# Optimization experiments

Hardware: AMD Instinct MI355X
Metric: run time of the kernel (lower is better)

Reference implementation:

```python
import jax, jax.numpy as jnp
import numpy as np

B, N, D, R, K = 16384, 20, 64, 3, 64  # batch, triples per sample, embed dim, n_relations, r_dim


def setup_inputs() -> dict:
    key = jax.random.key(0)
    ks = jax.random.split(key, 8)
    # xavier_normal std for [2D, K] matrices: sqrt(2/(2D+K))
    std_w = float(np.sqrt(2.0 / (2 * D + K)))
    std_r = float(np.sqrt(2.0 / (R + K)))
    return {
        "u_emb": jax.random.normal(ks[0], (B, D), dtype=jnp.float32),
        "i_emb": jax.random.normal(ks[1], (B, D), dtype=jnp.float32),
        "a_emb": jax.random.normal(ks[2], (B, N, D), dtype=jnp.float32),
        "o_emb": jax.random.normal(ks[3], (B, N, D), dtype=jnp.float32),
        "s": jax.random.randint(ks[4], (B, N), 0, R, dtype=jnp.int64),
        "w_uir": jax.random.normal(ks[5], (R, 2 * D, K), dtype=jnp.float32) * std_w,
        "w_aor": jax.random.normal(ks[6], (R, 2 * D, K), dtype=jnp.float32) * std_w,
        "r_vec": jax.random.normal(ks[7], (R, K), dtype=jnp.float32) * std_r,
    }


def reference(u_emb, i_emb, a_emb, o_emb, s, w_uir, w_aor, r_vec):
    # transr predictor, bpr loss
    ui_in = jnp.concatenate([u_emb, i_emb], axis=-1)          # [B, 2D]
    ao_in = jnp.concatenate([a_emb, o_emb], axis=-1)          # [B, N, 2D]
    n_rel = w_uir.shape[0]
    ui_emb = jnp.zeros(ao_in.shape[:2] + (w_uir.shape[-1],), dtype=ui_in.dtype)  # [B, N, K]
    ao_emb = jnp.zeros_like(ui_emb)
    for r_idx in range(n_rel):  # small fixed relation count
        m = (s == r_idx)[..., None]                            # [B, N, 1]
        ui_r = ui_in @ w_uir[r_idx] + r_vec[r_idx]             # [B, K]
        ao_r = jnp.einsum("bnd,dk->bnk", ao_in, w_aor[r_idx])  # [B, N, K]
        ui_emb = jnp.where(m, ui_r[:, None, :], ui_emb)
        ao_emb = jnp.where(m, ao_r, ao_emb)
    pred = jnp.sum(ui_emb * ao_emb, axis=-1)                   # [B, N]
    return pred
```

## Files before the change

kernel.cpp:

```cpp
#include <hip/hip_runtime.h>
#include <hip/hip_bf16.h>

#define BB   16384
#define NN   20
#define NREL 3

typedef __attribute__((ext_vector_type(8))) short  short8;
typedef __attribute__((ext_vector_type(4))) float  f32x4;

__device__ __forceinline__ float b2f(unsigned short v) {
    union { unsigned int u; float f; } x;
    x.u = ((unsigned int)v) << 16;
    return x.f;
}

__device__ __forceinline__ unsigned short f2bu(float f) {
    union { float f; unsigned int u; } x;
    x.f = f;
    unsigned int r = x.u + 0x7FFFu + ((x.u >> 16) & 1u);
    return (unsigned short)(r >> 16);
}

__global__ __launch_bounds__(256) void k_precompute(
    const float* __restrict__ w_uir,
    const float* __restrict__ w_aor,
    const float* __restrict__ r_vec,
    unsigned short* __restrict__ McatT,
    float* __restrict__ cvec)
{
    int idx = blockIdx.x * 256 + threadIdx.x;
    if (idx < NREL * 128 * 128) {
        int d = idx & 127;
        int e = (idx >> 7) & 127;
        int r = idx >> 14;
        const float4* pu = reinterpret_cast<const float4*>(w_uir + (r * 128 + d) * 64);
        const float4* pa = reinterpret_cast<const float4*>(w_aor + (r * 128 + e) * 64);
        float acc = 0.f;
        #pragma unroll
        for (int k = 0; k < 16; ++k) {
            float4 a = pu[k], b = pa[k];
            acc += a.x * b.x + a.y * b.y + a.z * b.z + a.w * b.w;
        }
        McatT[(r * 128 + e) * 128 + d] = f2bu(acc);
    } else if (idx < NREL * 128 * 128 + NREL * 128) {
        int j = idx - NREL * 128 * 128;
        int r = j >> 7, e = j & 127;
        const float4* pr = reinterpret_cast<const float4*>(r_vec + r * 64);
        const float4* pa = reinterpret_cast<const float4*>(w_aor + (r * 128 + e) * 64);
        float acc = 0.f;
        #pragma unroll
        for (int k = 0; k < 16; ++k) {
            float4 a = pr[k], b = pa[k];
            acc += a.x * b.x + a.y * b.y + a.z * b.z + a.w * b.w;
        }
        cvec[j] = acc;
    }
}

__global__ __launch_bounds__(256) void k_gemm(
    const float* __restrict__ u_emb,
    const float* __restrict__ i_emb,
    const unsigned short* __restrict__ McatT,
    const float* __restrict__ cvec,
    unsigned short* __restrict__ vp)
{
    __shared__ unsigned short Atile[64][136];
    const int t = threadIdx.x;
    const int bm = blockIdx.x & 255;
    const int bn = blockIdx.x >> 8;
    const int Mbase = bm * 64;
    const int Nbase = bn * 64;

    #pragma unroll
    for (int it = 0; it < 8; ++it) {
        int idx  = it * 256 + t;
        int row  = idx >> 5;
        int colg = idx & 31;
        const float* src = (colg < 16)
            ? (u_emb + (Mbase + row) * 64 + colg * 4)
            : (i_emb + (Mbase + row) * 64 + (colg - 16) * 4);
        float4 v = *reinterpret_cast<const float4*>(src);
        ushort4 h;
        h.x = f2bu(v.x); h.y = f2bu(v.y); h.z = f2bu(v.z); h.w = f2bu(v.w);
        *reinterpret_cast<ushort4*>(&Atile[row][colg * 4]) = h;
    }
    __syncthreads();

    const int w    = t >> 6;
    const int lane = t & 63;
    const int lr   = lane & 15;
    const int lk   = (lane >> 4) * 8;

    short8 afrag[4];
    #pragma unroll
    for (int kk = 0; kk < 4; ++kk)
        afrag[kk] = *reinterpret_cast<const short8*>(&Atile[w * 16 + lr][kk * 32 + lk]);

    #pragma unroll
    for (int nt = 0; nt < 4; ++nt) {
        f32x4 acc = {0.f, 0.f, 0.f, 0.f};
        int col = Nbase + nt * 16 + lr;
        #pragma unroll
        for (int kk = 0; kk < 4; ++kk) {
            short8 bfrag = *reinterpret_cast<const short8*>(McatT + col * 128 + kk * 32 + lk);
            acc = __builtin_amdgcn_mfma_f32_16x16x32_bf16(afrag[kk], bfrag, acc, 0, 0, 0);
        }
        float cb = cvec[col];
        #pragma unroll
        for (int reg = 0; reg < 4; ++reg) {
            int grow = Mbase + w * 16 + (lane >> 4) * 4 + reg;
            vp[grow * 384 + col] = f2bu(acc[reg] + cb);
        }
    }
}

__global__ __launch_bounds__(256) void k_pred(
    const float* __restrict__ a_emb,
    const float* __restrict__ o_emb,
    const int* __restrict__ s,
    const unsigned short* __restrict__ vp,
    float* __restrict__ out)
{
    int gt   = blockIdx.x * 256 + threadIdx.x;
    int trip = gt >> 4;
    int j    = gt & 15;
    int b    = trip / NN;

    float4 av = *reinterpret_cast<const float4*>(a_emb + trip * 64 + j * 4);
    float4 ov = *reinterpret_cast<const float4*>(o_emb + trip * 64 + j * 4);
    int sv = s[trip];
    const unsigned short* vb = vp + b * 384 + sv * 128;
    ushort4 v0 = *reinterpret_cast<const ushort4*>(vb + j * 4);
    ushort4 v1 = *reinterpret_cast<const ushort4*>(vb + 64 + j * 4);

    float sum = av.x * b2f(v0.x) + av.y * b2f(v0.y) + av.z * b2f(v0.z) + av.w * b2f(v0.w)
              + ov.x * b2f(v1.x) + ov.y * b2f(v1.y) + ov.z * b2f(v1.z) + ov.w * b2f(v1.w);
    sum += __shfl_xor(sum, 8, 64);
    sum += __shfl_xor(sum, 4, 64);
    sum += __shfl_xor(sum, 2, 64);
    sum += __shfl_xor(sum, 1, 64);
    if (j == 0)
        out[trip] = sum;
}

extern "C" void kernel_launch(void* const* d_in, const int* in_sizes, int n_in,
                              void* d_out, int out_size, void* d_ws, size_t ws_size,
                              hipStream_t stream) {
    const float* u_emb = (const float*)d_in[0];
    const float* i_emb = (const float*)d_in[1];
    const float* a_emb = (const float*)d_in[2];
    const float* o_emb = (const float*)d_in[3];
    const int*   s     = (const int*)d_in[4];
    const float* w_uir = (const float*)d_in[5];
    const float* w_aor = (const float*)d_in[6];
    const float* r_vec = (const float*)d_in[7];
    float* out = (float*)d_out;

    char* ws = (char*)d_ws;
    unsigned short* McatT = (unsigned short*)ws;
    float*          cvec  = (float*)(ws + 98304);
    unsigned short* vp    = (unsigned short*)(ws + 102400);

    k_precompute<<<194, 256, 0, stream>>>(w_uir, w_aor, r_vec, McatT, cvec);
    k_gemm<<<1536, 256, 0, stream>>>(u_emb, i_emb, McatT, cvec, vp);
    k_pred<<<20480, 256, 0, stream>>>(a_emb, o_emb, s, vp, out);
}
```

Baseline: 53.68 us.

## Stage prediction inputs into LDS via direct global-to-LDS loads with swizzled reads

The prediction kernel now has each block process 4 batch rows (80 triples). It bulk-copies the a/o embeddings and the matching vp rows into LDS with global_load_lds, then computes each dot product from LDS using an XOR-swizzled element index to avoid bank conflicts. The goal is fewer, larger memory transactions and lower per-thread launch overhead, since the grid drops from 20480 to 4096 blocks. The cost is about 44KB of LDS per block, which limits occupancy, plus a full wait before any compute starts.

Result: no change. 53.24 us (-0.8%).

```diff
diff --git a/kernel.cpp b/kernel.cpp
--- a/kernel.cpp
+++ b/kernel.cpp
@@ -8,10 +8,11 @@
 typedef __attribute__((ext_vector_type(8))) short  short8;
 typedef __attribute__((ext_vector_type(4))) float  f32x4;
 
-__device__ __forceinline__ float b2f(unsigned short v) {
-    union { unsigned int u; float f; } x;
-    x.u = ((unsigned int)v) << 16;
-    return x.f;
+__device__ __forceinline__ float lo16(unsigned int u) {
+    union { unsigned int x; float f; } c; c.x = u << 16; return c.f;
+}
+__device__ __forceinline__ float hi16(unsigned int u) {
+    union { unsigned int x; float f; } c; c.x = u & 0xFFFF0000u; return c.f;
 }
 
 __device__ __forceinline__ unsigned short f2bu(float f) {
@@ -114,6 +115,15 @@
     }
 }
 
+#define K3_G      4
+#define K3_TPB    (K3_G * NN)
+#define K3_BLOCKS (BB / K3_G)
+
+#define LDS_A   0
+#define LDS_O   20480
+#define LDS_VP  40960
+#define LDS_SZ  44032
+
 __global__ __launch_bounds__(256) void k_pred(
     const float* __restrict__ a_emb,
     const float* __restrict__ o_emb,
@@ -121,26 +131,78 @@
     const unsigned short* __restrict__ vp,
     float* __restrict__ out)
 {
-    int gt   = blockIdx.x * 256 + threadIdx.x;
-    int trip = gt >> 4;
-    int j    = gt & 15;
-    int b    = trip / NN;
-
-    float4 av = *reinterpret_cast<const float4*>(a_emb + trip * 64 + j * 4);
-    float4 ov = *reinterpret_cast<const float4*>(o_emb + trip * 64 + j * 4);
-    int sv = s[trip];
-    const unsigned short* vb = vp + b * 384 + sv * 128;
-    ushort4 v0 = *reinterpret_cast<const ushort4*>(vb + j * 4);
-    ushort4 v1 = *reinterpret_cast<const ushort4*>(vb + 64 + j * 4);
-
-    float sum = av.x * b2f(v0.x) + av.y * b2f(v0.y) + av.z * b2f(v0.z) + av.w * b2f(v0.w)
-              + ov.x * b2f(v1.x) + ov.y * b2f(v1.y) + ov.z * b2f(v1.z) + ov.w * b2f(v1.w);
-    sum += __shfl_xor(sum, 8, 64);
-    sum += __shfl_xor(sum, 4, 64);
-    sum += __shfl_xor(sum, 2, 64);
-    sum += __shfl_xor(sum, 1, 64);
-    if (j == 0)
-        out[trip] = sum;
+    __shared__ __align__(16) char lds[LDS_SZ];
+
+    const int tid  = threadIdx.x;
+    const int bid  = blockIdx.x;
+    const int wv   = tid >> 6;
+    const int lane = tid & 63;
+
+    const size_t t0 = (size_t)bid * K3_TPB;
+
+    const int g   = tid >> 4;
+    const int sub = tid & 15;
+    const int e4  = sub ^ (((lane >> 4) & 3) << 2);
+
+    const int sv0 = s[t0 +  0 + g];
+    const int sv1 = s[t0 + 16 + g];
+    const int sv2 = s[t0 + 32 + g];
+    const int sv3 = s[t0 + 48 + g];
+    const int sv4 = s[t0 + 64 + g];
+
+    {
+        const char* asrc = (const char*)(a_emb + t0 * 64);
+        const char* osrc = (const char*)(o_emb + t0 * 64);
+        const char* vsrc = (const char*)(vp + (size_t)bid * (K3_G * 3 * 128));
+        #pragma unroll
+        for (int i = 0; i < 5; ++i) {
+            int seg = i * 4 + wv;
+            __builtin_amdgcn_global_load_lds(
+                (const unsigned int*)(asrc + seg * 1024 + lane * 16),
+                (unsigned int*)(lds + LDS_A + seg * 1024), 16, 0, 0);
+        }
+        #pragma unroll
+        for (int i = 0; i < 5; ++i) {
+            int seg = i * 4 + wv;
+            __builtin_amdgcn_global_load_lds(
+                (const unsigned int*)(osrc + seg * 1024 + lane * 16),
+                (unsigned int*)(lds + LDS_O + seg * 1024), 16, 0, 0);
+        }
+        if (wv < 3) {
+            __builtin_amdgcn_global_load_lds(
+                (const unsigned int*)(vsrc + wv * 1024 + lane * 16),
+                (unsigned int*)(lds + LDS_VP + wv * 1024), 16, 0, 0);
+        }
+    }
+    asm volatile("s_waitcnt vmcnt(0)");
+    __syncthreads();
+
+    #define PASS(P, SV)                                                        \
+    {                                                                          \
+        const int ltrip = (P) * 16 + g;                                        \
+        const int bl    = ltrip / NN;                                          \
+        const int row   = bl * 3 + (SV);                                       \
+        float4 af = *(const float4*)(lds + LDS_A + ltrip * 256 + e4 * 16);     \
+        float4 of = *(const float4*)(lds + LDS_O + ltrip * 256 + e4 * 16);     \
+        uint2  wa = *(const uint2*)(lds + LDS_VP + row * 256 + e4 * 8);        \
+        uint2  wo = *(const uint2*)(lds + LDS_VP + row * 256 + 128 + e4 * 8);  \
+        float r = af.x * lo16(wa.x) + af.y * hi16(wa.x)                        \
+                + af.z * lo16(wa.y) + af.w * hi16(wa.y)                        \
+                + of.x * lo16(wo.x) + of.y * hi16(wo.x)                        \
+                + of.z * lo16(wo.y) + of.w * hi16(wo.y);                       \
+        r += __shfl_xor(r, 1, 64);                                             \
+        r += __shfl_xor(r, 2, 64);                                             \
+        r += __shfl_xor(r, 4, 64);                                             \
+        r += __shfl_xor(r, 8, 64);                                             \
+        if (sub == 0) out[t0 + ltrip] = r;                                     \
+    }
+
+    PASS(0, sv0)
+    PASS(1, sv1)
+    PASS(2, sv2)
+    PASS(3, sv3)
+    PASS(4, sv4)
+    #undef PASS
 }
 
 extern "C" void kernel_launch(void* const* d_in, const int* in_sizes, int n_in,
@@ -163,5 +225,5 @@
 
     k_precompute<<<194, 256, 0, stream>>>(w_uir, w_aor, r_vec, McatT, cvec);
     k_gemm<<<1536, 256, 0, stream>>>(u_emb, i_emb, McatT, cvec, vp);
-    k_pred<<<20480, 256, 0, stream>>>(a_emb, o_emb, s, vp, out);
-}
+    k_pred<<<K3_BLOCKS, 256, 0, stream>>>(a_emb, o_emb, s, vp, out);
+}
```

## Make k_pred persistent with double-buffered async global-to-LDS staging

Applied to the files above, without the earlier changes.

The prediction kernel becomes a persistent grid of 512 blocks. Each block walks 16 chunks of 40 triples (two batch rows each) and stages a/o embeddings, the per-row vp vectors and relation indices into a double-buffered LDS area using global_load_lds. It computes on the current buffer while the next chunk loads, with the aim of hiding memory latency and cutting the launch overhead of 20480 small blocks. In exchange there is a block-wide barrier every iteration, fewer resident blocks, and the staged s write may race with the following barrier's visibility of async loads.

Measured after the change: 54.43 us. No clear change (+1.4%).

```diff
diff --git a/kernel.cpp b/kernel.cpp
--- a/kernel.cpp
+++ b/kernel.cpp
@@ -8,10 +8,11 @@
 typedef __attribute__((ext_vector_type(8))) short  short8;
 typedef __attribute__((ext_vector_type(4))) float  f32x4;
 
-__device__ __forceinline__ float b2f(unsigned short v) {
-    union { unsigned int u; float f; } x;
-    x.u = ((unsigned int)v) << 16;
-    return x.f;
+__device__ __forceinline__ float lo16(unsigned int u) {
+    union { unsigned int x; float f; } c; c.x = u << 16; return c.f;
+}
+__device__ __forceinline__ float hi16(unsigned int u) {
+    union { unsigned int x; float f; } c; c.x = u & 0xFFFF0000u; return c.f;
 }
 
 __device__ __forceinline__ unsigned short f2bu(float f) {
@@ -114,6 +115,88 @@
     }
 }
 
+#define K3_BLOCKS 512
+#define K3_ITERS  16
+#define K3_TPS    40
+
+#define SL_A   0
+#define SL_O   10240
+#define SL_VP  20480
+#define SL_S   22016
+#define SL_SZ  22272
+
+__device__ __forceinline__ void k3_stage(
+    const float* __restrict__ a_emb, const float* __restrict__ o_emb,
+    const int* __restrict__ s, const unsigned short* __restrict__ vp,
+    char* L, int sidx, int wv, int lane)
+{
+    const size_t t0s = (size_t)sidx * K3_TPS;
+
+    int sval = 0;
+    if (wv == 2 && lane < K3_TPS) sval = s[t0s + lane];
+
+    const char* asrc = (const char*)(a_emb + t0s * 64);
+    const char* osrc = (const char*)(o_emb + t0s * 64);
+    const char* vsrc = (const char*)(vp + (size_t)sidx * (2 * 3 * 128));
+
+    if (wv < 2) {
+        #pragma unroll
+        for (int i = 0; i < 5; ++i) {
+            int seg = i * 2 + wv;
+            __builtin_amdgcn_global_load_lds(
+                (const unsigned int*)(asrc + seg * 1024 + (size_t)lane * 16),
+                (unsigned int*)(L + SL_A + seg * 1024), 16, 0, 0);
+        }
+    } else {
+        #pragma unroll
+        for (int i = 0; i < 5; ++i) {
+            int seg = i * 2 + (wv & 1);
+            __builtin_amdgcn_global_load_lds(
+                (const unsigned int*)(osrc + seg * 1024 + (size_t)lane * 16),
+                (unsigned int*)(L + SL_O + seg * 1024), 16, 0, 0);
+        }
+    }
+    if (wv == 3) {
+        __builtin_amdgcn_global_load_lds(
+            (const unsigned int*)(vsrc + (size_t)lane * 16),
+            (unsigned int*)(L + SL_VP), 16, 0, 0);
+        if (lane < 32)
+            __builtin_amdgcn_global_load_lds(
+                (const unsigned int*)(vsrc + 1024 + (size_t)lane * 16),
+                (unsigned int*)(L + SL_VP + 1024), 16, 0, 0);
+    }
+    if (wv == 2 && lane < K3_TPS)
+        *(int*)(L + SL_S + lane * 4) = sval;
+}
+
+__device__ __forceinline__ void k3_consume(
+    const char* L, int sidx, int g, int sub, float* __restrict__ out)
+{
+    const size_t t0s = (size_t)sidx * K3_TPS;
+    #pragma unroll
+    for (int p = 0; p < 3; ++p) {
+        const int ltrip = p * 16 + g;
+        if (p < 2 || g < 8) {
+            const int bl  = ltrip / NN;
+            const int sv  = *(const int*)(L + SL_S + ltrip * 4);
+            const int row = bl * 3 + sv;
+            float4 af = *(const float4*)(L + SL_A + ltrip * 256 + sub * 16);
+            float4 of = *(const float4*)(L + SL_O + ltrip * 256 + sub * 16);
+            uint2  wa = *(const uint2*)(L + SL_VP + row * 256 + sub * 8);
+            uint2  wo = *(const uint2*)(L + SL_VP + row * 256 + 128 + sub * 8);
+            float r = af.x * lo16(wa.x) + af.y * hi16(wa.x)
+                    + af.z * lo16(wa.y) + af.w * hi16(wa.y)
+                    + of.x * lo16(wo.x) + of.y * hi16(wo.x)
+                    + of.z * lo16(wo.y) + of.w * hi16(wo.y);
+            r += __shfl_xor(r, 1, 64);
+            r += __shfl_xor(r, 2, 64);
+            r += __shfl_xor(r, 4, 64);
+            r += __shfl_xor(r, 8, 64);
+            if (sub == 0) out[t0s + ltrip] = r;
+        }
+    }
+}
+
 __global__ __launch_bounds__(256) void k_pred(
     const float* __restrict__ a_emb,
     const float* __restrict__ o_emb,
@@ -121,26 +204,27 @@
     const unsigned short* __restrict__ vp,
     float* __restrict__ out)
 {
-    int gt   = blockIdx.x * 256 + threadIdx.x;
-    int trip = gt >> 4;
-    int j    = gt & 15;
-    int b    = trip / NN;
-
-    float4 av = *reinterpret_cast<const float4*>(a_emb + trip * 64 + j * 4);
-    float4 ov = *reinterpret_cast<const float4*>(o_emb + trip * 64 + j * 4);
-    int sv = s[trip];
-    const unsigned short* vb = vp + b * 384 + sv * 128;
-    ushort4 v0 = *reinterpret_cast<const ushort4*>(vb + j * 4);
-    ushort4 v1 = *reinterpret_cast<const ushort4*>(vb + 64 + j * 4);
-
-    float sum = av.x * b2f(v0.x) + av.y * b2f(v0.y) + av.z * b2f(v0.z) + av.w * b2f(v0.w)
-              + ov.x * b2f(v1.x) + ov.y * b2f(v1.y) + ov.z * b2f(v1.z) + ov.w * b2f(v1.w);
-    sum += __shfl_xor(sum, 8, 64);
-    sum += __shfl_xor(sum, 4, 64);
-    sum += __shfl_xor(sum, 2, 64);
-    sum += __shfl_xor(sum, 1, 64);
-    if (j == 0)
-        out[trip] = sum;
+    __shared__ __align__(16) char lds[2 * SL_SZ];
+
+    const int tid  = threadIdx.x;
+    const int wv   = tid >> 6;
+    const int lane = tid & 63;
+    const int bid  = blockIdx.x;
+    const int g    = tid >> 4;
+    const int sub  = tid & 15;
+
+    const int sbase = bid * K3_ITERS;
+
+    k3_stage(a_emb, o_emb, s, vp, lds, sbase, wv, lane);
+    __syncthreads();
+
+    for (int it = 0; it < K3_ITERS; ++it) {
+        if (it + 1 < K3_ITERS)
+            k3_stage(a_emb, o_emb, s, vp, lds + ((it + 1) & 1) * SL_SZ,
+                     sbase + it + 1, wv, lane);
+        k3_consume(lds + (it & 1) * SL_SZ, sbase + it, g, sub, out);
+        __syncthreads();
+    }
 }
 
 extern "C" void kernel_launch(void* const* d_in, const int* in_sizes, int n_in,
@@ -163,5 +247,5 @@
 
     k_precompute<<<194, 256, 0, stream>>>(w_uir, w_aor, r_vec, McatT, cvec);
     k_gemm<<<1536, 256, 0, stream>>>(u_emb, i_emb, McatT, cvec, vp);
-    k_pred<<<20480, 256, 0, stream>>>(a_emb, o_emb, s, vp, out);
-}
+    k_pred<<<K3_BLOCKS, 256, 0, stream>>>(a_emb, o_emb, s, vp, out);
+}
```
